# Optimization experiments

Hardware: AMD Instinct MI355X
Metric: run time of the kernel (lower is better)

The kernel has to match this reference:

```python
import jax, jax.numpy as jnp
import numpy as np

N, E = 50000, 800000
IN, HID, HEADS, OUT = 128, 64, 4, 32


def _lin_init(key, fin, fout):
    k1, k2 = jax.random.split(key)
    W = jax.random.normal(k1, (fin, fout), jnp.float32) / np.float32(np.sqrt(fin))
    b = jax.random.normal(k2, (fout,), jnp.float32) * 0.01
    return W, b


def setup_inputs() -> dict:
    key = jax.random.key(0)
    ks = jax.random.split(key, 12)
    x = jax.random.normal(ks[0], (N, IN), jnp.float32)
    edge_index = jax.random.randint(ks[1], (2, E), 0, N, dtype=jnp.int32)
    Wq1, bq1 = _lin_init(ks[2], IN, HEADS * HID)
    Wk1, bk1 = _lin_init(ks[3], IN, HEADS * HID)
    Wv1, bv1 = _lin_init(ks[4], IN, HEADS * HID)
    Ws1, bs1 = _lin_init(ks[5], IN, HID)  # skip: concat=False -> in -> hidden
    Wq2, bq2 = _lin_init(ks[6], HID, HEADS * HID)
    Wk2, bk2 = _lin_init(ks[7], HID, HEADS * HID)
    Wv2, bv2 = _lin_init(ks[8], HID, HEADS * HID)
    Ws2, bs2 = _lin_init(ks[9], HID, HID)
    ln_g = jnp.ones((HID,), jnp.float32)
    ln_b = jnp.zeros((HID,), jnp.float32)
    Wf, bf = _lin_init(ks[10], HID, OUT)
    return dict(x=x, edge_index=edge_index,
                Wq1=Wq1, bq1=bq1, Wk1=Wk1, bk1=bk1, Wv1=Wv1, bv1=bv1, Ws1=Ws1, bs1=bs1,
                Wq2=Wq2, bq2=bq2, Wk2=Wk2, bk2=bk2, Wv2=Wv2, bv2=bv2, Ws2=Ws2, bs2=bs2,
                ln_g=ln_g, ln_b=ln_b, Wf=Wf, bf=bf)


def transformer_conv(x, src, dst, Wq, bq, Wk, bk, Wv, bv, Ws, bs):
    """PyG TransformerConv, heads=HEADS, concat=False (head-mean), root_weight=True."""
    n = x.shape[0]
    q = (x @ Wq + bq).reshape(n, HEADS, HID)
    k = (x @ Wk + bk).reshape(n, HEADS, HID)
    v = (x @ Wv + bv).reshape(n, HEADS, HID)
    # per-edge attention logits: query at target (dst), key at source (src)
    logits = jnp.einsum('ehd,ehd->eh', q[dst], k[src]) / np.float32(np.sqrt(HID))  # [E,H]
    m = jax.ops.segment_max(logits, dst, num_segments=n)          # [N,H]
    e = jnp.exp(logits - m[dst])
    s = jax.ops.segment_sum(e, dst, num_segments=n)               # [N,H]
    alpha = e / s[dst]                                            # segment softmax
    agg = jax.ops.segment_sum(alpha[:, :, None] * v[src], dst, num_segments=n)  # [N,H,D]
    return agg.mean(axis=1) + (x @ Ws + bs)


def layernorm(x, g, b):
    mu = x.mean(-1, keepdims=True)
    var = x.var(-1, keepdims=True)
    return (x - mu) / jnp.sqrt(var + 1e-5) * g + b


def reference(x, edge_index, Wq1, bq1, Wk1, bk1, Wv1, bv1, Ws1, bs1,
              Wq2, bq2, Wk2, bk2, Wv2, bv2, Ws2, bs2, ln_g, ln_b, Wf, bf):
    src, dst = edge_index[0], edge_index[1]
    h = transformer_conv(x, src, dst, Wq1, bq1, Wk1, bk1, Wv1, bv1, Ws1, bs1)
    h = jax.nn.relu(layernorm(h, ln_g, ln_b))  # dropout = identity (eval)
    h = transformer_conv(h, src, dst, Wq2, bq2, Wk2, bk2, Wv2, bv2, Ws2, bs2)
    h = layernorm(h, ln_g, ln_b)  # k == num_layers-2: no relu/dropout
    return h @ Wf + bf
```

## Files before the change

### kernel.cpp

```cpp
#include <hip/hip_runtime.h>
#include <hip/hip_fp16.h>
#include <math.h>

#define NN 50000
#define EE 800000
#define HEADS 4
#define HIDD 64
#define OUTF 32
#define NXCD 8

struct __align__(8)  h4v { __half2 a, b; };
struct __align__(16) h8v { __half2 a, b, c, d; };

template<int KDIM>
__global__ __launch_bounds__(256) void qkvs_gemm(
    const float* __restrict__ X,
    const float* __restrict__ Wq, const float* __restrict__ bq,
    const float* __restrict__ Wk, const float* __restrict__ bk,
    const float* __restrict__ Wv, const float* __restrict__ bv,
    const float* __restrict__ Ws, const float* __restrict__ bs,
    float* __restrict__ Q, __half* __restrict__ KV, float* __restrict__ SKP)
{
    const int nwg = gridDim.x;
    const int i   = blockIdx.x;
    const int q8  = nwg >> 3, r8 = nwg & 7;
    const int xcd = i & 7, j = i >> 3;
    const int w   = (xcd < r8 ? xcd * (q8 + 1) : r8 * (q8 + 1) + (xcd - r8) * q8) + j;

    const int nt   = w % 13;
    const int row0 = (w / 13) * 128;

    const float* W; const float* bias; int mode, bcol, wstride;
    if (nt < 4)       { W = Wq; bias = bq; mode = 0; bcol = nt*64;     wstride = 256; }
    else if (nt < 8)  { W = Wk; bias = bk; mode = 1; bcol = (nt-4)*64; wstride = 256; }
    else if (nt < 12) { W = Wv; bias = bv; mode = 2; bcol = (nt-8)*64; wstride = 256; }
    else              { W = Ws; bias = bs; mode = 3; bcol = 0;         wstride = 64;  }

    __shared__ float sAT[32][132];
    __shared__ float sB[32][64];

    const int tid = threadIdx.x;
    const int tx = tid & 15, ty = tid >> 4;

    float acc[8][4] = {};

    for (int k0 = 0; k0 < KDIM; k0 += 32) {
        #pragma unroll
        for (int it = 0; it < 4; ++it) {
            int li = tid + 256*it;
            int r = li >> 3, c = li & 7;
            int gr = row0 + r;
            float4 a4 = {0.f,0.f,0.f,0.f};
            if (gr < NN) a4 = *(const float4*)&X[(size_t)gr*KDIM + k0 + c*4];
            sAT[c*4+0][r] = a4.x; sAT[c*4+1][r] = a4.y;
            sAT[c*4+2][r] = a4.z; sAT[c*4+3][r] = a4.w;
        }
        #pragma unroll
        for (int it = 0; it < 2; ++it) {
            int li = tid + 256*it;
            int kk = li >> 4, c4 = li & 15;
            *(float4*)&sB[kk][c4*4] =
                *(const float4*)&W[(size_t)(k0+kk)*wstride + bcol + c4*4];
        }
        __syncthreads();
        #pragma unroll
        for (int kk = 0; kk < 32; ++kk) {
            float4 a0 = *(const float4*)&sAT[kk][ty*8];
            float4 a1 = *(const float4*)&sAT[kk][ty*8+4];
            float4 b4 = *(const float4*)&sB[kk][tx*4];
            float a[8] = {a0.x,a0.y,a0.z,a0.w, a1.x,a1.y,a1.z,a1.w};
            float b[4] = {b4.x,b4.y,b4.z,b4.w};
            #pragma unroll
            for (int ii = 0; ii < 8; ++ii)
                #pragma unroll
                for (int jj = 0; jj < 4; ++jj)
                    acc[ii][jj] += a[ii]*b[jj];
        }
        __syncthreads();
    }

    const float4 bia = *(const float4*)&bias[bcol + tx*4];
    #pragma unroll
    for (int ii = 0; ii < 8; ++ii) {
        int gr = row0 + ty*8 + ii;
        if (gr >= NN) continue;
        float o0 = acc[ii][0] + bia.x, o1 = acc[ii][1] + bia.y;
        float o2 = acc[ii][2] + bia.z, o3 = acc[ii][3] + bia.w;
        if (mode == 0) {
            *(float4*)&Q[(size_t)gr*256 + bcol + tx*4] = {o0,o1,o2,o3};
        } else if (mode == 3) {
            *(float4*)&SKP[(size_t)gr*64 + tx*4] = {o0,o1,o2,o3};
        } else {
            h4v hh;
            hh.a = __floats2half2_rn(o0, o1);
            hh.b = __floats2half2_rn(o2, o3);
            int h = (mode == 1) ? nt-4 : nt-8;
            size_t base = (size_t)gr*512 + h*128 + tx*8 + (mode == 2 ? 4 : 0);
            *(h4v*)&KV[base] = hh;
        }
    }
}

__global__ __launch_bounds__(256) void hist_kernel(const int* __restrict__ dstA,
                                                   int* __restrict__ deg)
{
    int e = blockIdx.x * 256 + threadIdx.x;
    atomicAdd(&deg[dstA[e]], 1);
}

__global__ __launch_bounds__(1024) void scan_kernel(const int* __restrict__ deg,
                                                    int* __restrict__ rowptr,
                                                    int* __restrict__ cursor)
{
    __shared__ int sdata[1024];
    __shared__ int soff;
    const int tid = threadIdx.x;
    if (tid == 0) soff = 0;
    __syncthreads();
    for (int base = 0; base < NN; base += 1024) {
        int v = (base + tid < NN) ? deg[base + tid] : 0;
        sdata[tid] = v;
        __syncthreads();
        #pragma unroll
        for (int off = 1; off < 1024; off <<= 1) {
            int t = (tid >= off) ? sdata[tid - off] : 0;
            __syncthreads();
            sdata[tid] += t;
            __syncthreads();
        }
        int excl = sdata[tid] - v;
        if (base + tid < NN) {
            rowptr[base + tid] = soff + excl;
            cursor[base + tid] = soff + excl;
        }
        int total = sdata[1023];
        __syncthreads();
        if (tid == 0) soff += total;
        __syncthreads();
    }
    if (tid == 0) rowptr[NN] = EE;
}

__global__ __launch_bounds__(256) void scatter_kernel(const int* __restrict__ srcA,
                                                      const int* __restrict__ dstA,
                                                      int* __restrict__ cursor,
                                                      int* __restrict__ colidx)
{
    int e = blockIdx.x * 256 + threadIdx.x;
    int p = atomicAdd(&cursor[dstA[e]], 1);
    colidx[p] = srcA[e];
}

template<bool RELU>
__global__ __launch_bounds__(256) void node_attn(
    const int* __restrict__ rowptr, const int* __restrict__ colidx,
    const float* __restrict__ Q, const __half* __restrict__ KV,
    const float* __restrict__ SKP,
    const float* __restrict__ g, const float* __restrict__ b,
    float* __restrict__ Hout)
{
    int n = (blockIdx.x * blockDim.x + threadIdx.x) >> 6;
    if (n >= NN) return;
    const int lane = threadIdx.x & 63;
    const int h = lane >> 4, t = lane & 15;
    const int kvoff = h*128 + t*8;

    const float4 q4 = *(const float4*)&Q[(size_t)n*256 + h*64 + t*4];

    float4 acc = {0.f,0.f,0.f,0.f};
    float ssum = 0.f;
    const int e0 = rowptr[n], e1 = rowptr[n+1];
    int e = e0;
    for (; e + 2 <= e1; e += 2) {
        const int s0 = colidx[e], s1 = colidx[e+1];
        const h8v kv0 = *(const h8v*)&KV[(size_t)s0*512 + kvoff];
        const h8v kv1 = *(const h8v*)&KV[(size_t)s1*512 + kvoff];
        const float2 k0a = __half22float2(kv0.a), k0b = __half22float2(kv0.b);
        const float2 k1a = __half22float2(kv1.a), k1b = __half22float2(kv1.b);
        float p0 = q4.x*k0a.x + q4.y*k0a.y + q4.z*k0b.x + q4.w*k0b.y;
        float p1 = q4.x*k1a.x + q4.y*k1a.y + q4.z*k1b.x + q4.w*k1b.y;
        p0 += __shfl_xor(p0, 1);  p1 += __shfl_xor(p1, 1);
        p0 += __shfl_xor(p0, 2);  p1 += __shfl_xor(p1, 2);
        p0 += __shfl_xor(p0, 4);  p1 += __shfl_xor(p1, 4);
        p0 += __shfl_xor(p0, 8);  p1 += __shfl_xor(p1, 8);
        const float eh0 = __expf(p0 * 0.125f);
        const float eh1 = __expf(p1 * 0.125f);
        const float2 v0a = __half22float2(kv0.c), v0b = __half22float2(kv0.d);
        const float2 v1a = __half22float2(kv1.c), v1b = __half22float2(kv1.d);
        ssum  += eh0 + eh1;
        acc.x += eh0*v0a.x + eh1*v1a.x;
        acc.y += eh0*v0a.y + eh1*v1a.y;
        acc.z += eh0*v0b.x + eh1*v1b.x;
        acc.w += eh0*v0b.y + eh1*v1b.y;
    }
    for (; e < e1; ++e) {
        const int s = colidx[e];
        const h8v kv = *(const h8v*)&KV[(size_t)s*512 + kvoff];
        const float2 ka = __half22float2(kv.a), kb = __half22float2(kv.b);
        float p = q4.x*ka.x + q4.y*ka.y + q4.z*kb.x + q4.w*kb.y;
        p += __shfl_xor(p, 1);
        p += __shfl_xor(p, 2);
        p += __shfl_xor(p, 4);
        p += __shfl_xor(p, 8);
        const float eh = __expf(p * 0.125f);
        const float2 va = __half22float2(kv.c), vb = __half22float2(kv.d);
        ssum  += eh;
        acc.x += eh*va.x; acc.y += eh*va.y; acc.z += eh*vb.x; acc.w += eh*vb.y;
    }
    const float inv = (ssum != 0.f) ? 1.f/ssum : 0.f;
    acc.x *= inv; acc.y *= inv; acc.z *= inv; acc.w *= inv;

    #pragma unroll
    for (int o = 16; o < 64; o <<= 1) {
        acc.x += __shfl_xor(acc.x, o); acc.y += __shfl_xor(acc.y, o);
        acc.z += __shfl_xor(acc.z, o); acc.w += __shfl_xor(acc.w, o);
    }
    const float4 sk4 = *(const float4*)&SKP[(size_t)n*64 + t*4];
    float4 val;
    val.x = acc.x*0.25f + sk4.x; val.y = acc.y*0.25f + sk4.y;
    val.z = acc.z*0.25f + sk4.z; val.w = acc.w*0.25f + sk4.w;

    float m  = val.x + val.y + val.z + val.w;
    float m2 = val.x*val.x + val.y*val.y + val.z*val.z + val.w*val.w;
    #pragma unroll
    for (int o = 1; o < 16; o <<= 1) { m += __shfl_xor(m, o); m2 += __shfl_xor(m2, o); }
    m *= (1.f/64.f); m2 *= (1.f/64.f);
    const float rstd = rsqrtf(m2 - m*m + 1e-5f);
    const float4 g4 = *(const float4*)&g[t*4];
    const float4 b4 = *(const float4*)&b[t*4];
    float4 y;
    y.x = (val.x - m)*rstd*g4.x + b4.x;
    y.y = (val.y - m)*rstd*g4.y + b4.y;
    y.z = (val.z - m)*rstd*g4.z + b4.z;
    y.w = (val.w - m)*rstd*g4.w + b4.w;
    if (RELU) {
        y.x = fmaxf(y.x, 0.f); y.y = fmaxf(y.y, 0.f);
        y.z = fmaxf(y.z, 0.f); y.w = fmaxf(y.w, 0.f);
    }
    if (h == 0) *(float4*)&Hout[(size_t)n*64 + t*4] = y;
}

__global__ __launch_bounds__(256) void final_gemm(
    const float* __restrict__ H, const float* __restrict__ Wf,
    const float* __restrict__ bf, float* __restrict__ out)
{
    __shared__ float sW[64][32];
    __shared__ float sH[8][64];
    const int tid = threadIdx.x;
    #pragma unroll
    for (int i = 0; i < 8; ++i) {
        int li = tid + 256*i;
        sW[li >> 5][li & 31] = Wf[li];
    }
    const int n0 = blockIdx.x * 8;
    #pragma unroll
    for (int i = 0; i < 2; ++i) {
        int li = tid + 256*i;
        int r = li >> 6, d = li & 63;
        int gn = n0 + r;
        sH[r][d] = (gn < NN) ? H[(size_t)gn*64 + d] : 0.f;
    }
    __syncthreads();
    const int o = tid & 31, nl = tid >> 5;
    const int gn = n0 + nl;
    if (gn >= NN) return;
    float acc = bf[o];
    #pragma unroll
    for (int dd = 0; dd < 64; ++dd) acc += sH[nl][dd] * sW[dd][o];
    out[(size_t)gn*32 + o] = acc;
}

extern "C" void kernel_launch(void* const* d_in, const int* in_sizes, int n_in,
                              void* d_out, int out_size, void* d_ws, size_t ws_size,
                              hipStream_t stream) {
    const float* x   = (const float*)d_in[0];
    const int*   ei  = (const int*)d_in[1];
    const int* srcA = ei;
    const int* dstA = ei + EE;
    const float *Wq1=(const float*)d_in[2],  *bq1=(const float*)d_in[3];
    const float *Wk1=(const float*)d_in[4],  *bk1=(const float*)d_in[5];
    const float *Wv1=(const float*)d_in[6],  *bv1=(const float*)d_in[7];
    const float *Ws1=(const float*)d_in[8],  *bs1=(const float*)d_in[9];
    const float *Wq2=(const float*)d_in[10], *bq2=(const float*)d_in[11];
    const float *Wk2=(const float*)d_in[12], *bk2=(const float*)d_in[13];
    const float *Wv2=(const float*)d_in[14], *bv2=(const float*)d_in[15];
    const float *Ws2=(const float*)d_in[16], *bs2=(const float*)d_in[17];
    const float *ln_g=(const float*)d_in[18],*ln_b=(const float*)d_in[19];
    const float *Wf=(const float*)d_in[20],  *bf=(const float*)d_in[21];
    float* out = (float*)d_out;

    float* ws = (float*)d_ws;
    size_t off = 0;
    float* Q    = ws + off; off += (size_t)NN*256;
    __half* KV  = (__half*)(ws + off); off += (size_t)NN*256;
    float* SKP  = ws + off; off += (size_t)NN*64;
    float* H1   = ws + off; off += (size_t)NN*64;
    float* H2   = ws + off; off += (size_t)NN*64;
    int* deg    = (int*)(ws + off); off += NN;
    int* rowptr = (int*)(ws + off); off += NN + 1;
    int* cursor = (int*)(ws + off); off += NN;
    int* colidx = (int*)(ws + off); off += EE;

    const int rowTiles  = (NN + 127) / 128;
    const int gemmGrid  = 13 * rowTiles;
    const int edgeBlocks = EE / 256;
    const int nodeBlocks = NN / 4;

    hipMemsetAsync(deg, 0, NN * sizeof(int), stream);
    hist_kernel<<<edgeBlocks, 256, 0, stream>>>(dstA, deg);
    scan_kernel<<<1, 1024, 0, stream>>>(deg, rowptr, cursor);
    scatter_kernel<<<edgeBlocks, 256, 0, stream>>>(srcA, dstA, cursor, colidx);

    qkvs_gemm<128><<<gemmGrid, 256, 0, stream>>>(x, Wq1,bq1, Wk1,bk1, Wv1,bv1, Ws1,bs1,
                                                 Q, KV, SKP);
    node_attn<true><<<nodeBlocks, 256, 0, stream>>>(rowptr, colidx, Q, KV, SKP,
                                                    ln_g, ln_b, H1);

    qkvs_gemm<64><<<gemmGrid, 256, 0, stream>>>(H1, Wq2,bq2, Wk2,bk2, Wv2,bv2, Ws2,bs2,
                                                Q, KV, SKP);
    node_attn<false><<<nodeBlocks, 256, 0, stream>>>(rowptr, colidx, Q, KV, SKP,
                                                     ln_g, ln_b, H2);

    final_gemm<<<NN / 8, 256, 0, stream>>>(H2, Wf, bf, out);
}
```

Before: 743.2 us.

## Use fp16 MFMA matrix cores for the QKV/skip projection GEMM

Replaces the fp32 FMA register-tiled GEMM with MFMA 16x16x32 f16 instructions. The whole K dimension of A and B is staged once into LDS as fp16 (B transposed), and the row tile shrinks from 128 to 64, which doubles the grid. The aim is to move the projection GEMM onto the matrix units. In exchange, inputs and weights are rounded to fp16, which may reduce accuracy, and the epilogue now writes scalars instead of vectorized stores.

```diff
diff --git a/kernel.cpp b/kernel.cpp
--- a/kernel.cpp
+++ b/kernel.cpp
@@ -7,10 +7,13 @@
 #define HEADS 4
 #define HIDD 64
 #define OUTF 32
-#define NXCD 8
 
 struct __align__(8)  h4v { __half2 a, b; };
 struct __align__(16) h8v { __half2 a, b, c, d; };
+
+typedef __attribute__((ext_vector_type(8))) _Float16 f16x8;
+typedef __attribute__((ext_vector_type(4))) _Float16 f16x4;
+typedef __attribute__((ext_vector_type(4))) float    f32x4;
 
 template<int KDIM>
 __global__ __launch_bounds__(256) void qkvs_gemm(
@@ -21,6 +24,10 @@
     const float* __restrict__ Ws, const float* __restrict__ bs,
     float* __restrict__ Q, __half* __restrict__ KV, float* __restrict__ SKP)
 {
+    constexpr int KP = KDIM + 8;
+    __shared__ _Float16 Asm[64 * KP];
+    __shared__ _Float16 Bsm[64 * KP];
+
     const int nwg = gridDim.x;
     const int i   = blockIdx.x;
     const int q8  = nwg >> 3, r8 = nwg & 7;
@@ -28,7 +35,7 @@
     const int w   = (xcd < r8 ? xcd * (q8 + 1) : r8 * (q8 + 1) + (xcd - r8) * q8) + j;
 
     const int nt   = w % 13;
-    const int row0 = (w / 13) * 128;
+    const int row0 = (w / 13) * 64;
 
     const float* W; const float* bias; int mode, bcol, wstride;
     if (nt < 4)       { W = Wq; bias = bq; mode = 0; bcol = nt*64;     wstride = 256; }
@@ -36,67 +43,68 @@
     else if (nt < 12) { W = Wv; bias = bv; mode = 2; bcol = (nt-8)*64; wstride = 256; }
     else              { W = Ws; bias = bs; mode = 3; bcol = 0;         wstride = 64;  }
 
-    __shared__ float sAT[32][132];
-    __shared__ float sB[32][64];
-
     const int tid = threadIdx.x;
-    const int tx = tid & 15, ty = tid >> 4;
-
-    float acc[8][4] = {};
-
+
+    constexpr int AF4 = 64 * KDIM / 4;
+    #pragma unroll
+    for (int li = tid; li < AF4; li += 256) {
+        int r = li / (KDIM/4), c4 = li % (KDIM/4);
+        int gr = row0 + r;
+        float4 a4 = {0.f,0.f,0.f,0.f};
+        if (gr < NN) a4 = *(const float4*)&X[(size_t)gr*KDIM + c4*4];
+        f16x4 hv = { (_Float16)a4.x, (_Float16)a4.y, (_Float16)a4.z, (_Float16)a4.w };
+        *(f16x4*)&Asm[r*KP + c4*4] = hv;
+    }
+    constexpr int BF4 = KDIM * 16;
+    #pragma unroll
+    for (int li = tid; li < BF4; li += 256) {
+        int k = li >> 4, c4 = li & 15;
+        float4 wv4 = *(const float4*)&W[(size_t)k*wstride + bcol + c4*4];
+        Bsm[(c4*4+0)*KP + k] = (_Float16)wv4.x;
+        Bsm[(c4*4+1)*KP + k] = (_Float16)wv4.y;
+        Bsm[(c4*4+2)*KP + k] = (_Float16)wv4.z;
+        Bsm[(c4*4+3)*KP + k] = (_Float16)wv4.w;
+    }
+    __syncthreads();
+
+    const int lane = tid & 63, wvi = tid >> 6;
+    const int lr = lane & 15, lg = lane >> 4;
+    const int arow = wvi*16 + lr;
+
+    f32x4 acc[4];
+    #pragma unroll
+    for (int ci = 0; ci < 4; ++ci) acc[ci] = (f32x4){0.f,0.f,0.f,0.f};
+
+    #pragma unroll
     for (int k0 = 0; k0 < KDIM; k0 += 32) {
+        f16x8 af = *(const f16x8*)&Asm[arow*KP + k0 + lg*8];
         #pragma unroll
-        for (int it = 0; it < 4; ++it) {
-            int li = tid + 256*it;
-            int r = li >> 3, c = li & 7;
-            int gr = row0 + r;
-            float4 a4 = {0.f,0.f,0.f,0.f};
-            if (gr < NN) a4 = *(const float4*)&X[(size_t)gr*KDIM + k0 + c*4];
-            sAT[c*4+0][r] = a4.x; sAT[c*4+1][r] = a4.y;
-            sAT[c*4+2][r] = a4.z; sAT[c*4+3][r] = a4.w;
+        for (int ci = 0; ci < 4; ++ci) {
+            f16x8 bf = *(const f16x8*)&Bsm[(ci*16 + lr)*KP + k0 + lg*8];
+            acc[ci] = __builtin_amdgcn_mfma_f32_16x16x32_f16(af, bf, acc[ci], 0, 0, 0);
         }
+    }
+
+    #pragma unroll
+    for (int ci = 0; ci < 4; ++ci) {
+        const int col = ci*16 + lr;
+        const float bia = bias[bcol + col];
         #pragma unroll
-        for (int it = 0; it < 2; ++it) {
-            int li = tid + 256*it;
-            int kk = li >> 4, c4 = li & 15;
-            *(float4*)&sB[kk][c4*4] =
-                *(const float4*)&W[(size_t)(k0+kk)*wstride + bcol + c4*4];
-        }
-        __syncthreads();
-        #pragma unroll
-        for (int kk = 0; kk < 32; ++kk) {
-            float4 a0 = *(const float4*)&sAT[kk][ty*8];
-            float4 a1 = *(const float4*)&sAT[kk][ty*8+4];
-            float4 b4 = *(const float4*)&sB[kk][tx*4];
-            float a[8] = {a0.x,a0.y,a0.z,a0.w, a1.x,a1.y,a1.z,a1.w};
-            float b[4] = {b4.x,b4.y,b4.z,b4.w};
-            #pragma unroll
-            for (int ii = 0; ii < 8; ++ii)
-                #pragma unroll
-                for (int jj = 0; jj < 4; ++jj)
-                    acc[ii][jj] += a[ii]*b[jj];
-        }
-        __syncthreads();
-    }
-
-    const float4 bia = *(const float4*)&bias[bcol + tx*4];
-    #pragma unroll
-    for (int ii = 0; ii < 8; ++ii) {
-        int gr = row0 + ty*8 + ii;
-        if (gr >= NN) continue;
-        float o0 = acc[ii][0] + bia.x, o1 = acc[ii][1] + bia.y;
-        float o2 = acc[ii][2] + bia.z, o3 = acc[ii][3] + bia.w;
-        if (mode == 0) {
-            *(float4*)&Q[(size_t)gr*256 + bcol + tx*4] = {o0,o1,o2,o3};
-        } else if (mode == 3) {
-            *(float4*)&SKP[(size_t)gr*64 + tx*4] = {o0,o1,o2,o3};
-        } else {
-            h4v hh;
-            hh.a = __floats2half2_rn(o0, o1);
-            hh.b = __floats2half2_rn(o2, o3);
-            int h = (mode == 1) ? nt-4 : nt-8;
-            size_t base = (size_t)gr*512 + h*128 + tx*8 + (mode == 2 ? 4 : 0);
-            *(h4v*)&KV[base] = hh;
+        for (int ii = 0; ii < 4; ++ii) {
+            int gr = row0 + wvi*16 + lg*4 + ii;
+            if (gr >= NN) continue;
+            float o = acc[ci][ii] + bia;
+            if (mode == 0) {
+                Q[(size_t)gr*256 + bcol + col] = o;
+            } else if (mode == 3) {
+                SKP[(size_t)gr*64 + col] = o;
+            } else {
+                int h = bcol >> 6;
+                int d = col;
+                size_t idx = (size_t)gr*512 + h*128 + ((d>>2)<<3) + (d&3)
+                             + (mode == 2 ? 4 : 0);
+                KV[idx] = __float2half(o);
+            }
         }
     }
 }
@@ -301,7 +309,7 @@
     int* cursor = (int*)(ws + off); off += NN;
     int* colidx = (int*)(ws + off); off += EE;
 
-    const int rowTiles  = (NN + 127) / 128;
+    const int rowTiles  = (NN + 63) / 64;
     const int gemmGrid  = 13 * rowTiles;
     const int edgeBlocks = EE / 256;
     const int nodeBlocks = NN / 4;
```

Result: faster. 688.7 us (-7.3%).
